# Kernel optimization log

Measured on AMD Instinct MI355X. Metric: run time of the kernel, lower is better.

Reference implementation:

```python
import jax, jax.numpy as jnp
import numpy as np

N_EMBD = 1024
N_HEAD = 64

def setup_inputs() -> dict:
    key = jax.random.key(0)
    ks = jax.random.split(key, 7)
    B, T = 4, 4096
    x = jax.random.normal(ks[0], (B, T, N_EMBD), dtype=jnp.float32)
    # causal mask: True above the diagonal (masked positions)
    mask = jnp.triu(jnp.ones((T, T), dtype=bool), k=1)
    s = 1.0 / np.sqrt(N_EMBD)
    Wq = jax.random.normal(ks[1], (N_EMBD, N_HEAD), dtype=jnp.float32) * s
    bq = jnp.zeros((N_HEAD,), dtype=jnp.float32)
    Wk = jax.random.normal(ks[2], (N_EMBD, N_HEAD), dtype=jnp.float32) * s
    bk = jnp.zeros((N_HEAD,), dtype=jnp.float32)
    Wv = jax.random.normal(ks[3], (N_EMBD, N_HEAD), dtype=jnp.float32) * s
    bv = jnp.zeros((N_HEAD,), dtype=jnp.float32)
    return {"x": x, "mask": mask, "Wq": Wq, "bq": bq, "Wk": Wk, "bk": bk, "Wv": Wv, "bv": bv}

def reference(x, mask, Wq, bq, Wk, bk, Wv, bv):
    # x: [B,T,C], mask: [T,T] bool (True = masked)
    q = x @ Wq + bq            # [B,T,H]
    k = x @ Wk + bk            # [B,T,H]
    v = x @ Wv + bv            # [B,T,H]
    scale = 1.0 / jnp.sqrt(jnp.asarray(q.shape[-1], dtype=q.dtype))
    att = jnp.einsum('bth,bsh->bts', q, k) * scale   # [B,T,T]
    att = jnp.where(mask[None, :, :], -jnp.inf, att)
    att = jax.nn.softmax(att, axis=-1)
    # dropout omitted (eval mode / deterministic reference)
    return jnp.einsum('bts,bsh->bth', att, v)        # [B,T,H]
```

## Files before the change

### kernel.cpp

```cpp
#include <hip/hip_runtime.h>
#include <hip/hip_bf16.h>

#define BB 4
#define TT 4096
#define CC 1024
#define HH 64

typedef __attribute__((ext_vector_type(8))) short short8;
typedef __attribute__((ext_vector_type(4))) float floatx4;

__device__ __forceinline__ ushort f2bf(float f) {
    union { float f; unsigned u; } a; a.f = f;
    const unsigned u = a.u;
    return (ushort)((u + 0x7fffu + ((u >> 16) & 1u)) >> 16);
}
__device__ __forceinline__ float bf2f(ushort h) {
    union { unsigned u; float f; } a; a.u = ((unsigned)h) << 16; return a.f;
}

__global__ __launch_bounds__(256)
void wtrans_kernel(const float* __restrict__ Wq, const float* __restrict__ Wk,
                   const float* __restrict__ Wv, ushort* __restrict__ wT)
{
    const int mat = blockIdx.x >> 6;
    const int n   = blockIdx.x & 63;
    const float* W = (mat == 0) ? Wq : (mat == 1) ? Wk : Wv;
    ushort* dst = wT + ((size_t)mat * 64 + n) * 1024;
    for (int i = threadIdx.x; i < 1024; i += 256)
        dst[i] = f2bf(W[(size_t)i * 64 + n]);
}

__global__ __launch_bounds__(512)
void qkv_mfma_kernel(const float* __restrict__ x, const ushort* __restrict__ wT,
                     const float* __restrict__ bq, const float* __restrict__ bk,
                     const float* __restrict__ bv,
                     ushort* __restrict__ q, ushort* __restrict__ k,
                     ushort* __restrict__ vT)
{
    __shared__ ushort xs [32 * 72];
    __shared__ ushort ws_[192 * 72];

    const int tid = threadIdx.x, w = tid >> 6, lane = tid & 63;
    const int m = lane & 15, quad = lane >> 4;
    const int mt = w >> 2, nq = w & 3;
    const int row0 = blockIdx.x * 32;

    floatx4 acc[3];
    #pragma unroll
    for (int i = 0; i < 3; ++i) acc[i] = (floatx4){0.f, 0.f, 0.f, 0.f};

    for (int kc = 0; kc < 16; ++kc) {
        const int k0 = kc * 64;
        __syncthreads();
        {
            const int r = tid >> 4, seg = tid & 15;
            const float4 xv = *(const float4*)(x + (size_t)(row0 + r) * CC + k0 + seg * 4);
            ushort4 p; p.x = f2bf(xv.x); p.y = f2bf(xv.y); p.z = f2bf(xv.z); p.w = f2bf(xv.w);
            *(ushort4*)(xs + r * 72 + seg * 4) = p;
        }
        #pragma unroll
        for (int it = 0; it < 3; ++it) {
            const int t2 = it * 512 + tid;
            const int r = t2 >> 3, seg = t2 & 7;
            *(uint4*)(ws_ + r * 72 + seg * 8) = *(const uint4*)(wT + (size_t)r * 1024 + k0 + seg * 8);
        }
        __syncthreads();

        #pragma unroll
        for (int ks_ = 0; ks_ < 2; ++ks_) {
            const short8 a = *(const short8*)(xs + (mt * 16 + m) * 72 + ks_ * 32 + quad * 8);
            #pragma unroll
            for (int nt = 0; nt < 3; ++nt) {
                const short8 b_ = *(const short8*)(ws_ + (nq * 48 + nt * 16 + m) * 72 + ks_ * 32 + quad * 8);
                acc[nt] = __builtin_amdgcn_mfma_f32_16x16x32_bf16(a, b_, acc[nt], 0, 0, 0);
            }
        }
    }

    const int gr0 = row0 + mt * 16 + quad * 4;
    const int b = gr0 >> 12, t0 = gr0 & (TT - 1);
    #pragma unroll
    for (int nt = 0; nt < 3; ++nt) {
        const int gcol = nq * 48 + nt * 16 + m;
        const int mat = gcol >> 6, c = gcol & 63;
        const float bias = (mat == 0) ? bq[c] : (mat == 1) ? bk[c] : bv[c];
        if (mat == 0) {
            #pragma unroll
            for (int r = 0; r < 4; ++r)
                q[(size_t)(gr0 + r) * HH + c] = f2bf(acc[nt][r] + bias);
        } else if (mat == 1) {
            #pragma unroll
            for (int r = 0; r < 4; ++r)
                k[(size_t)(gr0 + r) * HH + c] = f2bf(acc[nt][r] + bias);
        } else {
            ushort4 pv;
            pv.x = f2bf(acc[nt][0] + bias); pv.y = f2bf(acc[nt][1] + bias);
            pv.z = f2bf(acc[nt][2] + bias); pv.w = f2bf(acc[nt][3] + bias);
            *(ushort4*)(vT + ((size_t)b * HH + c) * TT + t0) = pv;
        }
    }
}

__global__ __launch_bounds__(256)
void attn_mfma_kernel(const ushort* __restrict__ q, const ushort* __restrict__ k,
                      const ushort* __restrict__ vT,
                      float* __restrict__ partM, float* __restrict__ partL,
                      ushort* __restrict__ partO)
{
    __shared__ ushort qs[64 * 72];
    __shared__ ushort ks[64 * 72];
    __shared__ ushort vs[64 * 72];
    __shared__ ushort ps[4][16 * 72];

    const int tid = threadIdx.x, w = tid >> 6, lane = tid & 63;
    const int m = lane & 15, quad = lane >> 4;
    const int pid = blockIdx.x;
    const int job = pid >> 2, split = pid & 3;
    const int b = job >> 6, tile = job & 63;
    const int i0 = tile * 64;
    const int nch = tile + 1;
    const int lo = (nch * split) >> 2, hi = (nch * (split + 1)) >> 2;

    const size_t qbase = ((size_t)b * TT + i0) * HH;
    #pragma unroll
    for (int it = 0; it < 2; ++it) {
        const int t2 = it * 256 + tid;
        const int r = t2 >> 3, seg = t2 & 7;
        *(uint4*)(qs + r * 72 + seg * 8) = *(const uint4*)(q + qbase + (size_t)r * HH + seg * 8);
    }
    __syncthreads();

    const short8 aq0 = *(const short8*)(qs + (w * 16 + m) * 72 + quad * 8);
    const short8 aq1 = *(const short8*)(qs + (w * 16 + m) * 72 + 32 + quad * 8);

    float mrow[4], lrow[4];
    floatx4 oacc[4];
    #pragma unroll
    for (int r = 0; r < 4; ++r) { mrow[r] = -1e30f; lrow[r] = 0.f; }
    #pragma unroll
    for (int nt = 0; nt < 4; ++nt) oacc[nt] = (floatx4){0.f, 0.f, 0.f, 0.f};

    const int iq0 = i0 + w * 16;
    for (int ch = lo; ch < hi; ++ch) {
        const int s0 = ch * 64;
        __syncthreads();
        const size_t kb = ((size_t)b * TT + s0) * HH;
        #pragma unroll
        for (int it = 0; it < 2; ++it) {
            const int t2 = it * 256 + tid;
            const int r = t2 >> 3, seg = t2 & 7;
            *(uint4*)(ks + r * 72 + seg * 8) = *(const uint4*)(k + kb + (size_t)r * HH + seg * 8);
            *(uint4*)(vs + r * 72 + seg * 8) = *(const uint4*)(vT + ((size_t)b * HH + r) * TT + s0 + seg * 8);
        }
        __syncthreads();

        floatx4 sc[4];
        #pragma unroll
        for (int nt = 0; nt < 4; ++nt) {
            const short8 b0 = *(const short8*)(ks + (nt * 16 + m) * 72 + quad * 8);
            const short8 b1 = *(const short8*)(ks + (nt * 16 + m) * 72 + 32 + quad * 8);
            floatx4 s_ = (floatx4){0.f, 0.f, 0.f, 0.f};
            s_ = __builtin_amdgcn_mfma_f32_16x16x32_bf16(aq0, b0, s_, 0, 0, 0);
            s_ = __builtin_amdgcn_mfma_f32_16x16x32_bf16(aq1, b1, s_, 0, 0, 0);
            sc[nt] = s_;
        }

        #pragma unroll
        for (int r = 0; r < 4; ++r) {
            const int irow = iq0 + quad * 4 + r;
            float v0 = sc[0][r] * 0.125f, v1 = sc[1][r] * 0.125f;
            float v2 = sc[2][r] * 0.125f, v3 = sc[3][r] * 0.125f;
            if (s0      + m > irow) v0 = -1e30f;
            if (s0 + 16 + m > irow) v1 = -1e30f;
            if (s0 + 32 + m > irow) v2 = -1e30f;
            if (s0 + 48 + m > irow) v3 = -1e30f;
            float mx = fmaxf(fmaxf(v0, v1), fmaxf(v2, v3));
            mx = fmaxf(mx, __shfl_xor(mx, 1));
            mx = fmaxf(mx, __shfl_xor(mx, 2));
            mx = fmaxf(mx, __shfl_xor(mx, 4));
            mx = fmaxf(mx, __shfl_xor(mx, 8));
            const float mn = fmaxf(mrow[r], mx);
            const float alpha = __expf(mrow[r] - mn);
            mrow[r] = mn;
            v0 = __expf(v0 - mn); v1 = __expf(v1 - mn);
            v2 = __expf(v2 - mn); v3 = __expf(v3 - mn);
            float rs = v0 + v1 + v2 + v3;
            rs += __shfl_xor(rs, 1); rs += __shfl_xor(rs, 2);
            rs += __shfl_xor(rs, 4); rs += __shfl_xor(rs, 8);
            lrow[r] = lrow[r] * alpha + rs;
            oacc[0][r] *= alpha; oacc[1][r] *= alpha;
            oacc[2][r] *= alpha; oacc[3][r] *= alpha;
            ushort* pr = ps[w] + (quad * 4 + r) * 72;
            pr[m]      = f2bf(v0);
            pr[16 + m] = f2bf(v1);
            pr[32 + m] = f2bf(v2);
            pr[48 + m] = f2bf(v3);
        }

        #pragma unroll
        for (int ks_ = 0; ks_ < 2; ++ks_) {
            const short8 ap = *(const short8*)(ps[w] + m * 72 + ks_ * 32 + quad * 8);
            #pragma unroll
            for (int nt = 0; nt < 4; ++nt) {
                const short8 bv_ = *(const short8*)(vs + (nt * 16 + m) * 72 + ks_ * 32 + quad * 8);
                oacc[nt] = __builtin_amdgcn_mfma_f32_16x16x32_bf16(ap, bv_, oacc[nt], 0, 0, 0);
            }
        }
    }

    if (m == 0) {
        #pragma unroll
        for (int r = 0; r < 4; ++r) {
            const int row = w * 16 + quad * 4 + r;
            partM[(size_t)pid * 64 + row] = mrow[r];
            partL[(size_t)pid * 64 + row] = lrow[r];
        }
    }
    ushort* po = partO + ((size_t)pid * 64 + w * 16) * 64;
    #pragma unroll
    for (int r = 0; r < 4; ++r) {
        const int row = quad * 4 + r;
        #pragma unroll
        for (int nt = 0; nt < 4; ++nt)
            po[row * 64 + nt * 16 + m] = f2bf(oacc[nt][r]);
    }
}

__global__ __launch_bounds__(256)
void attn_combine_kernel(const float* __restrict__ partM, const float* __restrict__ partL,
                         const ushort* __restrict__ partO, float* __restrict__ out)
{
    const int job = blockIdx.x;
    const int tid = threadIdx.x;
    const int row = tid >> 2, dq = tid & 3;

    float m[4], l[4];
    #pragma unroll
    for (int s = 0; s < 4; ++s) {
        m[s] = partM[(size_t)(job * 4 + s) * 64 + row];
        l[s] = partL[(size_t)(job * 4 + s) * 64 + row];
    }
    const float M = fmaxf(fmaxf(m[0], m[1]), fmaxf(m[2], m[3]));
    float sc[4], L = 0.f;
    #pragma unroll
    for (int s = 0; s < 4; ++s) { sc[s] = __expf(m[s] - M); L += l[s] * sc[s]; }
    const float inv = 1.f / L;

    float o[16];
    #pragma unroll
    for (int i = 0; i < 16; ++i) o[i] = 0.f;
    #pragma unroll
    for (int s = 0; s < 4; ++s) {
        const ushort* po = partO + (((size_t)(job * 4 + s) * 64 + row) * 64 + dq * 16);
        #pragma unroll
        for (int i2 = 0; i2 < 2; ++i2) {
            const ushort4 pa = *(const ushort4*)(po + i2 * 8);
            const ushort4 pb = *(const ushort4*)(po + i2 * 8 + 4);
            o[i2*8+0] = fmaf(bf2f(pa.x), sc[s], o[i2*8+0]);
            o[i2*8+1] = fmaf(bf2f(pa.y), sc[s], o[i2*8+1]);
            o[i2*8+2] = fmaf(bf2f(pa.z), sc[s], o[i2*8+2]);
            o[i2*8+3] = fmaf(bf2f(pa.w), sc[s], o[i2*8+3]);
            o[i2*8+4] = fmaf(bf2f(pb.x), sc[s], o[i2*8+4]);
            o[i2*8+5] = fmaf(bf2f(pb.y), sc[s], o[i2*8+5]);
            o[i2*8+6] = fmaf(bf2f(pb.z), sc[s], o[i2*8+6]);
            o[i2*8+7] = fmaf(bf2f(pb.w), sc[s], o[i2*8+7]);
        }
    }
    float4* dst = (float4*)(out + ((size_t)job * 64 + row) * 64 + dq * 16);
    #pragma unroll
    for (int i = 0; i < 4; ++i) {
        float4 v; v.x = o[i*4]*inv; v.y = o[i*4+1]*inv; v.z = o[i*4+2]*inv; v.w = o[i*4+3]*inv;
        dst[i] = v;
    }
}

extern "C" void kernel_launch(void* const* d_in, const int* in_sizes, int n_in,
                              void* d_out, int out_size, void* d_ws, size_t ws_size,
                              hipStream_t stream) {
    (void)in_sizes; (void)n_in; (void)out_size; (void)ws_size;
    const float* x  = (const float*)d_in[0];
    const float* Wq = (const float*)d_in[2];
    const float* bq = (const float*)d_in[3];
    const float* Wk = (const float*)d_in[4];
    const float* bk = (const float*)d_in[5];
    const float* Wv = (const float*)d_in[6];
    const float* bv = (const float*)d_in[7];
    float* out = (float*)d_out;

    char* ws = (char*)d_ws;
    ushort* wT    = (ushort*)ws;
    ushort* qb    = (ushort*)(ws + 393216);
    ushort* kb    = qb + (size_t)BB * TT * HH;
    ushort* vTb   = kb + (size_t)BB * TT * HH;
    float*  partM = (float*) (ws + 6684672);
    float*  partL = (float*) (ws + 6946816);
    ushort* partO = (ushort*)(ws + 7208960);

    wtrans_kernel   <<<192, 256, 0, stream>>>(Wq, Wk, Wv, wT);
    qkv_mfma_kernel <<<(BB * TT) / 32, 512, 0, stream>>>(x, wT, bq, bk, bv, qb, kb, vTb);
    attn_mfma_kernel<<<BB * 64 * 4, 256, 0, stream>>>(qb, kb, vTb, partM, partL, partO);
    attn_combine_kernel<<<BB * 64, 256, 0, stream>>>(partM, partL, partO, out);
}
```

Before: 225.7 us.

## Load QKV projection operands directly from global memory, tile the weight transpose

The QKV projection kernel drops its LDS staging and __syncthreads, so each wave loads its x fragment (converted to bf16 in registers) and its weight fragments straight from global memory into MFMA operands. Blocks shrink to 16 rows and 256 threads, each wave covering 48 output columns. The weight transpose kernel now goes through an LDS tile so its global reads and writes are coalesced. In exchange, the four waves of a block each reload the same x rows, and weight reuse now relies on the cache instead of shared memory.

```diff
diff --git a/kernel.cpp b/kernel.cpp
--- a/kernel.cpp
+++ b/kernel.cpp
@@ -22,81 +22,89 @@
 void wtrans_kernel(const float* __restrict__ Wq, const float* __restrict__ Wk,
                    const float* __restrict__ Wv, ushort* __restrict__ wT)
 {
-    const int mat = blockIdx.x >> 6;
-    const int n   = blockIdx.x & 63;
+    __shared__ ushort tile[64 * 72];
+    const int tid = threadIdx.x;
+    const int mat = blockIdx.x >> 4, kt = blockIdx.x & 15;
     const float* W = (mat == 0) ? Wq : (mat == 1) ? Wk : Wv;
-    ushort* dst = wT + ((size_t)mat * 64 + n) * 1024;
-    for (int i = threadIdx.x; i < 1024; i += 256)
-        dst[i] = f2bf(W[(size_t)i * 64 + n]);
-}
-
-__global__ __launch_bounds__(512)
+    #pragma unroll
+    for (int it = 0; it < 16; ++it) {
+        const int idx = it * 256 + tid;
+        const int r = idx >> 6, c = idx & 63;
+        tile[c * 72 + r] = f2bf(W[(size_t)(kt * 64 + r) * 64 + c]);
+    }
+    __syncthreads();
+    #pragma unroll
+    for (int it = 0; it < 16; ++it) {
+        const int idx = it * 256 + tid;
+        const int n = idx >> 6, kk = idx & 63;
+        wT[((size_t)mat * 64 + n) * 1024 + kt * 64 + kk] = tile[n * 72 + kk];
+    }
+}
+
+__global__ __launch_bounds__(256)
 void qkv_mfma_kernel(const float* __restrict__ x, const ushort* __restrict__ wT,
                      const float* __restrict__ bq, const float* __restrict__ bk,
                      const float* __restrict__ bv,
                      ushort* __restrict__ q, ushort* __restrict__ k,
                      ushort* __restrict__ vT)
 {
-    __shared__ ushort xs [32 * 72];
-    __shared__ ushort ws_[192 * 72];
-
     const int tid = threadIdx.x, w = tid >> 6, lane = tid & 63;
     const int m = lane & 15, quad = lane >> 4;
-    const int mt = w >> 2, nq = w & 3;
-    const int row0 = blockIdx.x * 32;
+    const int row0 = blockIdx.x * 16;
 
     floatx4 acc[3];
     #pragma unroll
     for (int i = 0; i < 3; ++i) acc[i] = (floatx4){0.f, 0.f, 0.f, 0.f};
 
+    const float*  xp = x  + (size_t)(row0 + m) * CC + quad * 8;
+    const ushort* wp = wT + (size_t)(w * 48 + m) * 1024 + quad * 8;
+
+    #pragma unroll 2
     for (int kc = 0; kc < 16; ++kc) {
         const int k0 = kc * 64;
-        __syncthreads();
-        {
-            const int r = tid >> 4, seg = tid & 15;
-            const float4 xv = *(const float4*)(x + (size_t)(row0 + r) * CC + k0 + seg * 4);
-            ushort4 p; p.x = f2bf(xv.x); p.y = f2bf(xv.y); p.z = f2bf(xv.z); p.w = f2bf(xv.w);
-            *(ushort4*)(xs + r * 72 + seg * 4) = p;
-        }
-        #pragma unroll
-        for (int it = 0; it < 3; ++it) {
-            const int t2 = it * 512 + tid;
-            const int r = t2 >> 3, seg = t2 & 7;
-            *(uint4*)(ws_ + r * 72 + seg * 8) = *(const uint4*)(wT + (size_t)r * 1024 + k0 + seg * 8);
-        }
-        __syncthreads();
-
-        #pragma unroll
-        for (int ks_ = 0; ks_ < 2; ++ks_) {
-            const short8 a = *(const short8*)(xs + (mt * 16 + m) * 72 + ks_ * 32 + quad * 8);
+        short8 a[2];
+        #pragma unroll
+        for (int h = 0; h < 2; ++h) {
+            const float4 f0 = *(const float4*)(xp + k0 + h * 32);
+            const float4 f1 = *(const float4*)(xp + k0 + h * 32 + 4);
+            short8 av;
+            av[0] = (short)f2bf(f0.x); av[1] = (short)f2bf(f0.y);
+            av[2] = (short)f2bf(f0.z); av[3] = (short)f2bf(f0.w);
+            av[4] = (short)f2bf(f1.x); av[5] = (short)f2bf(f1.y);
+            av[6] = (short)f2bf(f1.z); av[7] = (short)f2bf(f1.w);
+            a[h] = av;
+        }
+        #pragma unroll
+        for (int h = 0; h < 2; ++h) {
             #pragma unroll
-            for (int nt = 0; nt < 3; ++nt) {
-                const short8 b_ = *(const short8*)(ws_ + (nq * 48 + nt * 16 + m) * 72 + ks_ * 32 + quad * 8);
-                acc[nt] = __builtin_amdgcn_mfma_f32_16x16x32_bf16(a, b_, acc[nt], 0, 0, 0);
+            for (int j = 0; j < 3; ++j) {
+                const short8 bfrag = *(const short8*)(wp + (size_t)j * 16 * 1024 + k0 + h * 32);
+                acc[j] = __builtin_amdgcn_mfma_f32_16x16x32_bf16(a[h], bfrag, acc[j], 0, 0, 0);
             }
         }
     }
 
-    const int gr0 = row0 + mt * 16 + quad * 4;
-    const int b = gr0 >> 12, t0 = gr0 & (TT - 1);
-    #pragma unroll
-    for (int nt = 0; nt < 3; ++nt) {
-        const int gcol = nq * 48 + nt * 16 + m;
-        const int mat = gcol >> 6, c = gcol & 63;
+    const int gr0 = row0 + quad * 4;
+    const int b_ = gr0 >> 12, t0 = gr0 & (TT - 1);
+    #pragma unroll
+    for (int j = 0; j < 3; ++j) {
+        const int nt = w * 3 + j;
+        const int mat = nt >> 2;
+        const int c = (nt & 3) * 16 + m;
         const float bias = (mat == 0) ? bq[c] : (mat == 1) ? bk[c] : bv[c];
         if (mat == 0) {
             #pragma unroll
             for (int r = 0; r < 4; ++r)
-                q[(size_t)(gr0 + r) * HH + c] = f2bf(acc[nt][r] + bias);
+                q[(size_t)(gr0 + r) * HH + c] = f2bf(acc[j][r] + bias);
         } else if (mat == 1) {
             #pragma unroll
             for (int r = 0; r < 4; ++r)
-                k[(size_t)(gr0 + r) * HH + c] = f2bf(acc[nt][r] + bias);
+                k[(size_t)(gr0 + r) * HH + c] = f2bf(acc[j][r] + bias);
         } else {
             ushort4 pv;
-            pv.x = f2bf(acc[nt][0] + bias); pv.y = f2bf(acc[nt][1] + bias);
-            pv.z = f2bf(acc[nt][2] + bias); pv.w = f2bf(acc[nt][3] + bias);
-            *(ushort4*)(vT + ((size_t)b * HH + c) * TT + t0) = pv;
+            pv.x = f2bf(acc[j][0] + bias); pv.y = f2bf(acc[j][1] + bias);
+            pv.z = f2bf(acc[j][2] + bias); pv.w = f2bf(acc[j][3] + bias);
+            *(ushort4*)(vT + ((size_t)b_ * HH + c) * TT + t0) = pv;
         }
     }
 }
@@ -296,8 +304,8 @@
     float*  partL = (float*) (ws + 6946816);
     ushort* partO = (ushort*)(ws + 7208960);
 
-    wtrans_kernel   <<<192, 256, 0, stream>>>(Wq, Wk, Wv, wT);
-    qkv_mfma_kernel <<<(BB * TT) / 32, 512, 0, stream>>>(x, wT, bq, bk, bv, qb, kb, vTb);
+    wtrans_kernel   <<<48, 256, 0, stream>>>(Wq, Wk, Wv, wT);
+    qkv_mfma_kernel <<<(BB * TT) / 16, 256, 0, stream>>>(x, wT, bq, bk, bv, qb, kb, vTb);
     attn_mfma_kernel<<<BB * 64 * 4, 256, 0, stream>>>(qb, kb, vTb, partM, partL, partO);
     attn_combine_kernel<<<BB * 64, 256, 0, stream>>>(partM, partL, partO, out);
 }
```

Result: slower. 267.6 us (+18.5%).
